# Kernel optimization log

Measured on AMD Instinct MI355X. Metric: run time of the kernel, lower is better.

## Reference

```python
import jax, jax.numpy as jnp
import numpy as np

H = 1024      # hidden_size
NH = 16       # num_attention_heads
KV = 4        # num_key_value_heads
HD = 64       # head_dim
E = 16        # num_experts
K = 2         # num_experts_per_tok
F = 1024      # moe_intermediate_size
EPS = 1e-6
THETA = 10000.0
B, S = 2, 1024


def rmsnorm(x, w):
    v = x.astype(jnp.float32)
    v = v * jax.lax.rsqrt(jnp.mean(v * v, axis=-1, keepdims=True) + EPS)
    return (v * w).astype(x.dtype)


def rotate_half(x):
    h = x.shape[-1] // 2
    return jnp.concatenate([-x[..., h:], x[..., :h]], axis=-1)


def setup_inputs() -> dict:
    key = jax.random.key(0)
    ks = jax.random.split(key, 12)
    s = 0.02
    return {
        "hidden_states": jax.random.normal(ks[0], (B, S, H), jnp.float32),
        "position_ids": jnp.broadcast_to(jnp.arange(S, dtype=jnp.int32), (B, S)),
        "ln1_w": jnp.ones((H,), jnp.float32),
        "ln2_w": jnp.ones((H,), jnp.float32),
        "q_w": jax.random.normal(ks[1], (NH * HD, H), jnp.float32) * s,
        "k_w": jax.random.normal(ks[2], (KV * HD, H), jnp.float32) * s,
        "v_w": jax.random.normal(ks[3], (KV * HD, H), jnp.float32) * s,
        "o_w": jax.random.normal(ks[4], (H, NH * HD), jnp.float32) * s,
        "qn_w": jnp.ones((HD,), jnp.float32),
        "kn_w": jnp.ones((HD,), jnp.float32),
        "gate_w": jax.random.normal(ks[5], (E, H), jnp.float32) * s,
        "w_gate": jax.random.normal(ks[6], (E, F, H), jnp.float32) * s,
        "w_up": jax.random.normal(ks[7], (E, F, H), jnp.float32) * s,
        "w_down": jax.random.normal(ks[8], (E, H, F), jnp.float32) * s,
    }


def reference(hidden_states, position_ids, ln1_w, ln2_w, q_w, k_w, v_w, o_w,
              qn_w, kn_w, gate_w, w_gate, w_up, w_down):
    b, s, _ = hidden_states.shape
    # ---- attention (pre-norm, bidirectional, GQA, RoPE, q/k RMSNorm) ----
    h = rmsnorm(hidden_states, ln1_w)
    q = (h @ q_w.T).reshape(b, s, NH, HD)
    k = (h @ k_w.T).reshape(b, s, KV, HD)
    v = (h @ v_w.T).reshape(b, s, KV, HD)
    q = jnp.swapaxes(rmsnorm(q, qn_w), 1, 2)   # [b,NH,s,HD]
    k = jnp.swapaxes(rmsnorm(k, kn_w), 1, 2)   # [b,KV,s,HD]
    v = jnp.swapaxes(v, 1, 2)
    inv_freq = 1.0 / (THETA ** (jnp.arange(0, HD, 2, dtype=jnp.float32) / HD))
    freqs = position_ids.astype(jnp.float32)[..., None] * inv_freq  # [b,s,HD/2]
    emb = jnp.concatenate([freqs, freqs], axis=-1)                  # [b,s,HD]
    cos = jnp.cos(emb)[:, None]                                     # [b,1,s,HD]
    sin = jnp.sin(emb)[:, None]
    q = q * cos + rotate_half(q) * sin
    k = k * cos + rotate_half(k) * sin
    rep = NH // KV
    k = jnp.repeat(k, rep, axis=1)
    v = jnp.repeat(v, rep, axis=1)
    scores = jnp.einsum('bhqd,bhkd->bhqk', q, k) * (HD ** -0.5)
    attn = jax.nn.softmax(scores.astype(jnp.float32), axis=-1).astype(q.dtype)
    o = jnp.einsum('bhqk,bhkd->bhqd', attn, v)
    o = jnp.swapaxes(o, 1, 2).reshape(b, s, NH * HD) @ o_w.T
    x1 = hidden_states + o
    # ---- sparse MoE (pre-norm, top-k routing, silu-gated experts) ----
    h2 = rmsnorm(x1, ln2_w)
    xf = h2.reshape(-1, H)                                  # [T,H]
    logits = xf @ gate_w.T                                  # [T,E]
    probs = jax.nn.softmax(logits.astype(jnp.float32), axis=-1)
    w, sel = jax.lax.top_k(probs, K)                        # [T,K]
    w = w / jnp.sum(w, axis=-1, keepdims=True)              # norm_topk_prob
    T = xf.shape[0]
    # combine weights scattered into dense [T,E] (zero for unselected experts)
    cw = jnp.zeros((T, E), jnp.float32).at[jnp.arange(T)[:, None], sel].add(w)
    g = jnp.einsum('th,efh->tef', xf, w_gate)
    u = jnp.einsum('th,efh->tef', xf, w_up)
    a = jax.nn.silu(g) * u
    y = jnp.einsum('tef,ehf,te->th', a, w_down, cw.astype(xf.dtype))
    out = x1 + y.reshape(b, s, H)
    return out, logits.reshape(b, s, E)
```

## Files before the change

kernel.cpp:

```cpp
#include <hip/hip_runtime.h>
#include <hip/hip_bf16.h>
#include <math.h>

typedef __bf16 bf16x8 __attribute__((ext_vector_type(8)));
typedef float f32x4 __attribute__((ext_vector_type(4)));

constexpr int HID = 1024;
constexpr int NHEAD = 16;
constexpr int NKV = 4;
constexpr int HDIM = 64;
constexpr int NEXP = 16;
constexpr int FFD = 1024;
constexpr int NB = 2;
constexpr int SEQ = 1024;
constexpr int TOK = NB * SEQ;
constexpr int QKV_N = NHEAD * HDIM + 2 * NKV * HDIM;
constexpr float RMS_EPS = 1e-6f;
constexpr int LDP = 32;
constexpr int PL = 64 * LDP;
constexpr int MAXBLK = 2 * TOK / 64 + NEXP;

__device__ __forceinline__ int swz(int row, int e8) {
  return row * LDP + (e8 ^ (((row >> 1) & 3) << 3));
}

__device__ __forceinline__ void split2(float x, __bf16& h1, __bf16& h2) {
  h1 = (__bf16)x;
  h2 = (__bf16)(x - (float)h1);
}

__device__ __forceinline__ void mfma_step3(const __bf16* sm, int wr, int wc,
                                           int lm, int lq, f32x4 (&acc)[2][2]) {
  int ao0 = swz(wr + lm, lq * 8), ao1 = ao0 + 16 * LDP;
  int bo0 = swz(wc + lm, lq * 8), bo1 = bo0 + 16 * LDP;
  bf16x8 a10 = *(const bf16x8*)(sm + ao0),          a11 = *(const bf16x8*)(sm + ao1);
  bf16x8 a20 = *(const bf16x8*)(sm + PL + ao0),     a21 = *(const bf16x8*)(sm + PL + ao1);
  bf16x8 b10 = *(const bf16x8*)(sm + 2 * PL + bo0), b11 = *(const bf16x8*)(sm + 2 * PL + bo1);
  bf16x8 b20 = *(const bf16x8*)(sm + 3 * PL + bo0), b21 = *(const bf16x8*)(sm + 3 * PL + bo1);
#define MF(A, B, i, j) acc[i][j] = __builtin_amdgcn_mfma_f32_16x16x32_bf16(A, B, acc[i][j], 0, 0, 0)
  MF(a10, b10, 0, 0); MF(a10, b11, 0, 1); MF(a11, b10, 1, 0); MF(a11, b11, 1, 1);
  MF(a10, b20, 0, 0); MF(a10, b21, 0, 1); MF(a11, b20, 1, 0); MF(a11, b21, 1, 1);
  MF(a20, b10, 0, 0); MF(a20, b11, 0, 1); MF(a21, b10, 1, 0); MF(a21, b11, 1, 1);
#undef MF
}

__device__ __forceinline__ void cvt8(__bf16* dst, float4 f0, float4 f1) {
  __bf16 tmp[8] __attribute__((aligned(16))) = {
      (__bf16)f0.x, (__bf16)f0.y, (__bf16)f0.z, (__bf16)f0.w,
      (__bf16)f1.x, (__bf16)f1.y, (__bf16)f1.z, (__bf16)f1.w};
  *(int4*)dst = *(const int4*)tmp;
}


__global__ __launch_bounds__(256) void split2_kernel(
    const float* __restrict__ src, __bf16* __restrict__ p1,
    __bf16* __restrict__ p2, int n) {
  int i = (blockIdx.x * 256 + threadIdx.x) * 4;
  if (i >= n) return;
  float4 v = *(const float4*)(src + i);
  __bf16 t1[4] __attribute__((aligned(8))), t2[4] __attribute__((aligned(8)));
  split2(v.x, t1[0], t2[0]);
  split2(v.y, t1[1], t2[1]);
  split2(v.z, t1[2], t2[2]);
  split2(v.w, t1[3], t2[3]);
  *(int2*)(p1 + i) = *(const int2*)t1;
  *(int2*)(p2 + i) = *(const int2*)t2;
}

__global__ __launch_bounds__(256) void rmsnorm_split2_kernel(
    const float* __restrict__ x, const float* __restrict__ w,
    __bf16* __restrict__ p1, __bf16* __restrict__ p2) {
  int row = blockIdx.x;
  const float* xr = x + (size_t)row * HID;
  float4 v = ((const float4*)xr)[threadIdx.x];
  float ss = v.x * v.x + v.y * v.y + v.z * v.z + v.w * v.w;
  for (int off = 32; off; off >>= 1) ss += __shfl_xor(ss, off);
  __shared__ float red[4];
  int lane = threadIdx.x & 63, wid = threadIdx.x >> 6;
  if (lane == 0) red[wid] = ss;
  __syncthreads();
  float tot = red[0] + red[1] + red[2] + red[3];
  float scale = rsqrtf(tot / (float)HID + RMS_EPS);
  float4 wv = ((const float4*)w)[threadIdx.x];
  float o[4] = {v.x * scale * wv.x, v.y * scale * wv.y,
                v.z * scale * wv.z, v.w * scale * wv.w};
  __bf16 t1[4] __attribute__((aligned(8))), t2[4] __attribute__((aligned(8)));
#pragma unroll
  for (int i = 0; i < 4; i++) split2(o[i], t1[i], t2[i]);
  size_t idx = (size_t)row * HID + threadIdx.x * 4;
  *(int2*)(p1 + idx) = *(const int2*)t1;
  *(int2*)(p2 + idx) = *(const int2*)t2;
}

__global__ __launch_bounds__(256) void rmsnorm_dual_kernel(
    const float* __restrict__ x, const float* __restrict__ w,
    float* __restrict__ outf, __bf16* __restrict__ outb) {
  int row = blockIdx.x;
  const float* xr = x + (size_t)row * HID;
  float4 v = ((const float4*)xr)[threadIdx.x];
  float ss = v.x * v.x + v.y * v.y + v.z * v.z + v.w * v.w;
  for (int off = 32; off; off >>= 1) ss += __shfl_xor(ss, off);
  __shared__ float red[4];
  int lane = threadIdx.x & 63, wid = threadIdx.x >> 6;
  if (lane == 0) red[wid] = ss;
  __syncthreads();
  float tot = red[0] + red[1] + red[2] + red[3];
// ... 7 lines not shown
#pragma unroll
  for (int i = 0; i < 4; i++) tb[i] = (__bf16)o[i];
  *(int2*)(outb + idx) = *(const int2*)tb;
}

__global__ __launch_bounds__(256) void rope_split_kernel(
    const float* __restrict__ qkv, const int* __restrict__ pos_ids,
    const float* __restrict__ qn_w, const float* __restrict__ kn_w,
    __bf16* __restrict__ qp1, __bf16* __restrict__ qp2,
    __bf16* __restrict__ kp1, __bf16* __restrict__ kp2,
    __bf16* __restrict__ vp1, __bf16* __restrict__ vp2) {
  int t = blockIdx.x;
  int b = t >> 10, s = t & 1023;
  int lane = threadIdx.x & 63, w = threadIdx.x >> 6;
  float pos = (float)pos_ids[t];
  int fi = lane & 31;
  float inv = powf(10000.0f, -((float)(2 * fi)) / 64.0f);
  float cs = cosf(pos * inv), sn = sinf(pos * inv);
  for (int i = 0; i < 6; i++) {
    int hh = w + 4 * i;
    float val = qkv[(size_t)t * QKV_N + hh * 64 + lane];
    __bf16 h1, h2;
    if (hh < 20) {
      float ss = val * val;
      for (int off = 32; off; off >>= 1) ss += __shfl_xor(ss, off);
      float scale = rsqrtf(ss / 64.0f + RMS_EPS);
      float wgt = (hh < 16) ? qn_w[lane] : kn_w[lane];
      val = val * scale * wgt;
      float partner = __shfl_xor(val, 32);
      float rot = (lane < 32) ? -partner : partner;
      val = val * cs + rot * sn;
      split2(val, h1, h2);
      if (hh < 16) {
        size_t idx = (((size_t)b * NHEAD + hh) * SEQ + s) * HDIM + lane;
        qp1[idx] = h1; qp2[idx] = h2;
      } else {
        size_t idx = (((size_t)b * NKV + (hh - 16)) * SEQ + s) * HDIM + lane;
        kp1[idx] = h1; kp2[idx] = h2;
      }
    } else {
      split2(val, h1, h2);
      size_t idx = (((size_t)b * NKV + (hh - 20)) * HDIM + lane) * SEQ + s;
      vp1[idx] = h1; vp2[idx] = h2;
    }
  }
}

__global__ __launch_bounds__(256) void softmax2_kernel(
    const float* __restrict__ sf,
    __bf16* __restrict__ p1, __bf16* __restrict__ p2) {
  size_t roff = (size_t)blockIdx.x * SEQ;
  int tid = threadIdx.x;
  float4 v4 = *(const float4*)(sf + roff + tid * 4);
  float v[4] = {v4.x, v4.y, v4.z, v4.w};
  float mx = fmaxf(fmaxf(v[0], v[1]), fmaxf(v[2], v[3]));
  for (int off = 32; off; off >>= 1) mx = fmaxf(mx, __shfl_xor(mx, off));
  __shared__ float red[4], red2[4];
  int lane = tid & 63, wid = tid >> 6;
  if (lane == 0) red[wid] = mx;
  __syncthreads();
  mx = fmaxf(fmaxf(red[0], red[1]), fmaxf(red[2], red[3]));
  float e[4], sum = 0.f;
#pragma unroll
  for (int i = 0; i < 4; i++) { e[i] = expf(v[i] - mx); sum += e[i]; }
  for (int off = 32; off; off >>= 1) sum += __shfl_xor(sum, off);
  if (lane == 0) red2[wid] = sum;
  __syncthreads();
  sum = red2[0] + red2[1] + red2[2] + red2[3];
  float invs = 1.0f / sum;
  __bf16 t1[4] __attribute__((aligned(8))), t2[4] __attribute__((aligned(8)));
#pragma unroll
  for (int i = 0; i < 4; i++) split2(e[i] * invs, t1[i], t2[i]);
  *(int2*)(p1 + roff + tid * 4) = *(const int2*)t1;
  *(int2*)(p2 + roff + tid * 4) = *(const int2*)t2;
}


__global__ __launch_bounds__(256) void gemm_qkv4(
    const __bf16* __restrict__ a1, const __bf16* __restrict__ a2,
    const __bf16* __restrict__ b1, const __bf16* __restrict__ b2,
    float* __restrict__ qkv) {
  int m0 = blockIdx.x * 64, n0 = blockIdx.y * 64;
  __shared__ __bf16 sm[2][4 * PL];
  int tid = threadIdx.x, r = tid >> 2, c8 = (tid & 3) * 8;
  size_t aoff = (size_t)(m0 + r) * HID + c8, boff = (size_t)(n0 + r) * HID + c8;
  f32x4 acc[2][2] = {};
  int lane = tid & 63, wid = tid >> 6;
  int wr = (wid >> 1) * 32, wc = (wid & 1) * 32, lq = lane >> 4, lm = lane & 15;
  int sidx = swz(r, c8);
  int4 rA1, rA2, rA3, rA4, rB1, rB2, rB3, rB4;
  auto preloadA = [&](int k0) {
    rA1 = *(const int4*)(a1 + aoff + k0); rA2 = *(const int4*)(a2 + aoff + k0);
    rA3 = *(const int4*)(b1 + boff + k0); rA4 = *(const int4*)(b2 + boff + k0);
  };
  auto preloadB = [&](int k0) {
    rB1 = *(const int4*)(a1 + aoff + k0); rB2 = *(const int4*)(a2 + aoff + k0);
    rB3 = *(const int4*)(b1 + boff + k0); rB4 = *(const int4*)(b2 + boff + k0);
  };
  auto stageA = [&](int p) {
    *(int4*)&sm[p][0 * PL + sidx] = rA1; *(int4*)&sm[p][1 * PL + sidx] = rA2;
    *(int4*)&sm[p][2 * PL + sidx] = rA3; *(int4*)&sm[p][3 * PL + sidx] = rA4;
  };
  auto stageB = [&](int p) {
    *(int4*)&sm[p][0 * PL + sidx] = rB1; *(int4*)&sm[p][1 * PL + sidx] = rB2;
    *(int4*)&sm[p][2 * PL + sidx] = rB3; *(int4*)&sm[p][3 * PL + sidx] = rB4;
  };
  preloadA(0); stageA(0);
  preloadA(32); preloadB(64);
  __syncthreads();
  int p = 0;
  for (int k0 = 0; k0 < HID; k0 += 64) {
    if (k0 + 32 < HID) stageA(p ^ 1);
    if (k0 + 96 < HID) preloadA(k0 + 96);
    mfma_step3(sm[p], wr, wc, lm, lq, acc);
    __syncthreads(); p ^= 1;
    if (k0 + 64 < HID) stageB(p ^ 1);
    if (k0 + 128 < HID) preloadB(k0 + 128);
    mfma_step3(sm[p], wr, wc, lm, lq, acc);
    __syncthreads(); p ^= 1;
  }
#pragma unroll
  for (int mt = 0; mt < 2; mt++)
#pragma unroll
    for (int nt = 0; nt < 2; nt++)
#pragma unroll
      for (int i = 0; i < 4; i++) {
        int gm = m0 + wr + mt * 16 + lq * 4 + i;
        int gc = n0 + wc + nt * 16 + lm;
        qkv[(size_t)gm * QKV_N + gc] = acc[mt][nt][i];
      }
}

__global__ __launch_bounds__(256) void gemm_scores4(
    const __bf16* __restrict__ qp1, const __bf16* __restrict__ qp2,
    const __bf16* __restrict__ kp1, const __bf16* __restrict__ kp2,
    float* __restrict__ sf, int b, int h0) {
  int hz = blockIdx.z, h = h0 + hz;
  int m0 = blockIdx.x * 64, n0 = blockIdx.y * 64;
  size_t qbase = ((size_t)(b * NHEAD + h)) * SEQ * HDIM;
  size_t kbase = ((size_t)(b * NKV + (h >> 2))) * SEQ * HDIM;
  __shared__ __bf16 sm[4 * PL];
  int tid = threadIdx.x, r = tid >> 2, c8 = (tid & 3) * 8;
  size_t aoff = qbase + (size_t)(m0 + r) * HDIM + c8;
  size_t boff = kbase + (size_t)(n0 + r) * HDIM + c8;
  f32x4 acc[2][2] = {};
  int lane = tid & 63, wid = tid >> 6;
  int wr = (wid >> 1) * 32, wc = (wid & 1) * 32, lq = lane >> 4, lm = lane & 15;
  int sidx = swz(r, c8);
  int4 ra1, ra2, rb1, rb2;
  auto preload = [&](int k0) {
    ra1 = *(const int4*)(qp1 + aoff + k0);
    ra2 = *(const int4*)(qp2 + aoff + k0);
    rb1 = *(const int4*)(kp1 + boff + k0);
    rb2 = *(const int4*)(kp2 + boff + k0);
  };
  auto stage = [&]() {
    *(int4*)&sm[0 * PL + sidx] = ra1;
    *(int4*)&sm[1 * PL + sidx] = ra2;
    *(int4*)&sm[2 * PL + sidx] = rb1;
    *(int4*)&sm[3 * PL + sidx] = rb2;
  };
  preload(0); stage();
  for (int k0 = 0; k0 < HDIM; k0 += 32) {
    __syncthreads();
    if (k0 + 32 < HDIM) preload(k0 + 32);
    mfma_step3(sm, wr, wc, lm, lq, acc);
    __syncthreads();
    if (k0 + 32 < HDIM) stage();
  }
#pragma unroll
  for (int mt = 0; mt < 2; mt++)
#pragma unroll
    for (int nt = 0; nt < 2; nt++)
#pragma unroll
      for (int i = 0; i < 4; i++) {
        int gm = m0 + wr + mt * 16 + lq * 4 + i;
        int gc = n0 + wc + nt * 16 + lm;
        size_t idx = ((size_t)hz * SEQ + gm) * SEQ + gc;
        sf[idx] = acc[mt][nt][i] * 0.125f;
      }
}

__global__ __launch_bounds__(256) void gemm_pv4(
    const __bf16* __restrict__ s1, const __bf16* __restrict__ s2,
    const __bf16* __restrict__ vp1, const __bf16* __restrict__ vp2,
    __bf16* __restrict__ o1, __bf16* __restrict__ o2,
    int b, int h0) {
  int hz = blockIdx.z, h = h0 + hz;
  int m0 = blockIdx.x * 64;
  size_t pbase = (size_t)hz * SEQ * SEQ;
  size_t vbase = ((size_t)(b * NKV + (h >> 2))) * HDIM * SEQ;
  __shared__ __bf16 sm[2][4 * PL];
  int tid = threadIdx.x, r = tid >> 2, c8 = (tid & 3) * 8;
  size_t aoff = pbase + (size_t)(m0 + r) * SEQ + c8;
  size_t boff = vbase + (size_t)r * SEQ + c8;
  f32x4 acc[2][2] = {};
  int lane = tid & 63, wid = tid >> 6;
  int wr = (wid >> 1) * 32, wc = (wid & 1) * 32, lq = lane >> 4, lm = lane & 15;
  int sidx = swz(r, c8);
  int4 rA1, rA2, rA3, rA4, rB1, rB2, rB3, rB4;
  auto preloadA = [&](int k0) {
    rA1 = *(const int4*)(s1 + aoff + k0);  rA2 = *(const int4*)(s2 + aoff + k0);
    rA3 = *(const int4*)(vp1 + boff + k0); rA4 = *(const int4*)(vp2 + boff + k0);
  };
  auto preloadB = [&](int k0) {
    rB1 = *(const int4*)(s1 + aoff + k0);  rB2 = *(const int4*)(s2 + aoff + k0);
    rB3 = *(const int4*)(vp1 + boff + k0); rB4 = *(const int4*)(vp2 + boff + k0);
  };
  auto stageA = [&](int p) {
    *(int4*)&sm[p][0 * PL + sidx] = rA1; *(int4*)&sm[p][1 * PL + sidx] = rA2;
    *(int4*)&sm[p][2 * PL + sidx] = rA3; *(int4*)&sm[p][3 * PL + sidx] = rA4;
  };
  auto stageB = [&](int p) {
    *(int4*)&sm[p][0 * PL + sidx] = rB1; *(int4*)&sm[p][1 * PL + sidx] = rB2;
    *(int4*)&sm[p][2 * PL + sidx] = rB3; *(int4*)&sm[p][3 * PL + sidx] = rB4;
  };
  preloadA(0); stageA(0);
  preloadA(32); preloadB(64);
  __syncthreads();
  int p = 0;
  for (int k0 = 0; k0 < SEQ; k0 += 64) {
    if (k0 + 32 < SEQ) stageA(p ^ 1);
    if (k0 + 96 < SEQ) preloadA(k0 + 96);
    mfma_step3(sm[p], wr, wc, lm, lq, acc);
    __syncthreads(); p ^= 1;
    if (k0 + 64 < SEQ) stageB(p ^ 1);
    if (k0 + 128 < SEQ) preloadB(k0 + 128);
    mfma_step3(sm[p], wr, wc, lm, lq, acc);
    __syncthreads(); p ^= 1;
  }
#pragma unroll
  for (int mt = 0; mt < 2; mt++)
#pragma unroll
    for (int nt = 0; nt < 2; nt++)
#pragma unroll
      for (int i = 0; i < 4; i++) {
        int gm = m0 + wr + mt * 16 + lq * 4 + i;
        int gc = wc + nt * 16 + lm;
        size_t idx = ((size_t)(b * SEQ + gm)) * HID + h * 64 + gc;
        __bf16 h1_, h2_;
        split2(acc[mt][nt][i], h1_, h2_);
        o1[idx] = h1_; o2[idx] = h2_;
      }
}

__global__ __launch_bounds__(256) void gemm_oproj4(
    const __bf16* __restrict__ a1, const __bf16* __restrict__ a2,
    const __bf16* __restrict__ b1, const __bf16* __restrict__ b2,
    const float* __restrict__ hidden, float* __restrict__ x1, float* __restrict__ outp) {
  int m0 = blockIdx.x * 64, n0 = blockIdx.y * 64;
  __shared__ __bf16 sm[2][4 * PL];
  int tid = threadIdx.x, r = tid >> 2, c8 = (tid & 3) * 8;
  size_t aoff = (size_t)(m0 + r) * HID + c8, boff = (size_t)(n0 + r) * HID + c8;
  f32x4 acc[2][2] = {};
  int lane = tid & 63, wid = tid >> 6;
  int wr = (wid >> 1) * 32, wc = (wid & 1) * 32, lq = lane >> 4, lm = lane & 15;
  int sidx = swz(r, c8);
  int4 rA1, rA2, rA3, rA4, rB1, rB2, rB3, rB4;
  auto preloadA = [&](int k0) {
    rA1 = *(const int4*)(a1 + aoff + k0); rA2 = *(const int4*)(a2 + aoff + k0);
    rA3 = *(const int4*)(b1 + boff + k0); rA4 = *(const int4*)(b2 + boff + k0);
  };
  auto preloadB = [&](int k0) {
    rB1 = *(const int4*)(a1 + aoff + k0); rB2 = *(const int4*)(a2 + aoff + k0);
    rB3 = *(const int4*)(b1 + boff + k0); rB4 = *(const int4*)(b2 + boff + k0);
  };
  auto stageA = [&](int p) {
    *(int4*)&sm[p][0 * PL + sidx] = rA1; *(int4*)&sm[p][1 * PL + sidx] = rA2;
    *(int4*)&sm[p][2 * PL + sidx] = rA3; *(int4*)&sm[p][3 * PL + sidx] = rA4;
  };
  auto stageB = [&](int p) {
    *(int4*)&sm[p][0 * PL + sidx] = rB1; *(int4*)&sm[p][1 * PL + sidx] = rB2;
    *(int4*)&sm[p][2 * PL + sidx] = rB3; *(int4*)&sm[p][3 * PL + sidx] = rB4;
  };
  preloadA(0); stageA(0);
  preloadA(32); preloadB(64);
  __syncthreads();
  int p = 0;
  for (int k0 = 0; k0 < HID; k0 += 64) {
    if (k0 + 32 < HID) stageA(p ^ 1);
    if (k0 + 96 < HID) preloadA(k0 + 96);
    mfma_step3(sm[p], wr, wc, lm, lq, acc);
    __syncthreads(); p ^= 1;
    if (k0 + 64 < HID) stageB(p ^ 1);
    if (k0 + 128 < HID) preloadB(k0 + 128);
    mfma_step3(sm[p], wr, wc, lm, lq, acc);
    __syncthreads(); p ^= 1;
  }
#pragma unroll
  for (int mt = 0; mt < 2; mt++)
#pragma unroll
    for (int nt = 0; nt < 2; nt++)
#pragma unroll
      for (int i = 0; i < 4; i++) {
        int gm = m0 + wr + mt * 16 + lq * 4 + i;
        int gc = n0 + wc + nt * 16 + lm;
        size_t idx = (size_t)gm * HID + gc;
        float val = hidden[idx] + acc[mt][nt][i];
        x1[idx] = val;
        outp[idx] = val;
      }
}


__global__ void zero_cnt_kernel(int* cnt) {
  if (threadIdx.x < NEXP) cnt[threadIdx.x] = 0;
}

__global__ __launch_bounds__(64) void gating_kernel(
    const float* __restrict__ h2f, const float* __restrict__ gw,
    float* __restrict__ logits_out, int* __restrict__ cnt,
    int* __restrict__ list, float* __restrict__ wt) {
  int t = blockIdx.x;
  int lane = threadIdx.x;
  const float* xr = h2f + (size_t)t * HID;
  float part[NEXP] = {};
  for (int k = lane; k < HID; k += 64) {
    float xv = xr[k];
#pragma unroll
    for (int e = 0; e < NEXP; e++) part[e] += xv * gw[e * HID + k];
  }
#pragma unroll
  for (int e = 0; e < NEXP; e++)
    for (int off = 32; off; off >>= 1) part[e] += __shfl_xor(part[e], off);
  if (lane < NEXP) logits_out[(size_t)t * NEXP + lane] = part[lane];
  float mx = part[0];
#pragma unroll
  for (int e = 1; e < NEXP; e++) mx = fmaxf(mx, part[e]);
  float pe[NEXP];
#pragma unroll
  for (int e = 0; e < NEXP; e++) pe[e] = expf(part[e] - mx);
  int e0 = 0; float p0 = pe[0];
#pragma unroll
  for (int e = 1; e < NEXP; e++) if (pe[e] > p0) { p0 = pe[e]; e0 = e; }
  int e1 = -1; float p1 = -1.f;
#pragma unroll
  for (int e = 0; e < NEXP; e++) if (e != e0 && pe[e] > p1) { p1 = pe[e]; e1 = e; }
  float wsum = p0 + p1;
  if (lane == 0) {
    int pos0 = atomicAdd(&cnt[e0], 1);
    list[e0 * TOK + pos0] = t;
    wt[e0 * TOK + pos0] = p0 / wsum;
    int pos1 = atomicAdd(&cnt[e1], 1);
    list[e1 * TOK + pos1] = t;
    wt[e1 * TOK + pos1] = p1 / wsum;
  }
}

__global__ void scan_kernel(const int* __restrict__ cnt, int* __restrict__ base,
                            int* __restrict__ btab, int* __restrict__ nblk) {
  if (threadIdx.x == 0 && blockIdx.x == 0) {
    int acc = 0, nb = 0;
    for (int e = 0; e < NEXP; e++) {
      base[e] = acc; acc += cnt[e];
      for (int m0 = 0; m0 < cnt[e]; m0 += 64) {
        btab[2 * nb] = e; btab[2 * nb + 1] = m0; nb++;
      }
    }
    base[NEXP] = acc;
    *nblk = nb;
  }
}

__global__ __launch_bounds__(256) void gemm_gateup3(
    const __bf16* __restrict__ h2, const float* __restrict__ w_gate,
    const float* __restrict__ w_up, const int* __restrict__ cnt,
    const int* __restrict__ base, const int* __restrict__ list,
    const int* __restrict__ btab, const int* __restrict__ nblk,
    __bf16* __restrict__ aws) {
  int slot = blockIdx.y;
  if (slot >= *nblk) return;
  int e = btab[2 * slot], m0 = btab[2 * slot + 1];
  int ce = cnt[e];
  int n0 = blockIdx.x * 64;
  int be = base[e];
  __shared__ __bf16 As[2][PL], Bg[2][PL], Bu[2][PL];
  int tid = threadIdx.x, r = tid >> 2, c8 = (tid & 3) * 8;
  int ridx = m0 + r; if (ridx >= ce) ridx = ce - 1;
  const __bf16* arow = h2 + (size_t)list[e * TOK + ridx] * HID + c8;
  const float* bgrow = w_gate + ((size_t)e * FFD + n0 + r) * HID + c8;
  const float* burow = w_up + ((size_t)e * FFD + n0 + r) * HID + c8;
  int lane = tid & 63, wid = tid >> 6;
  int wr = (wid >> 1) * 32, wc = (wid & 1) * 32, lq = lane >> 4, lm = lane & 15;
  int sidx = swz(r, c8);
  f32x4 ag[2][2] = {}, au[2][2] = {};
  int4 raA, raB; float4 rgA0, rgA1, ruA0, ruA1, rgB0, rgB1, ruB0, ruB1;
  auto preloadA = [&](int k0) {
    raA = *(const int4*)(arow + k0);
    rgA0 = *(const float4*)(bgrow + k0); rgA1 = *(const float4*)(bgrow + k0 + 4);
    ruA0 = *(const float4*)(burow + k0); ruA1 = *(const float4*)(burow + k0 + 4);
  };
  auto preloadB = [&](int k0) {
    raB = *(const int4*)(arow + k0);
    rgB0 = *(const float4*)(bgrow + k0); rgB1 = *(const float4*)(bgrow + k0 + 4);
    ruB0 = *(const float4*)(burow + k0); ruB1 = *(const float4*)(burow + k0 + 4);
  };
  auto stageA = [&](int p) {
    *(int4*)&As[p][sidx] = raA;
    cvt8(&Bg[p][sidx], rgA0, rgA1);
    cvt8(&Bu[p][sidx], ruA0, ruA1);
  };
  auto stageB = [&](int p) {
    *(int4*)&As[p][sidx] = raB;
    cvt8(&Bg[p][sidx], rgB0, rgB1);
    cvt8(&Bu[p][sidx], ruB0, ruB1);
  };
  auto compute = [&](int p) {
    int ao0 = swz(wr + lm, lq * 8), ao1 = ao0 + 16 * LDP;
    int bo0 = swz(wc + lm, lq * 8), bo1 = bo0 + 16 * LDP;
    bf16x8 a0 = *(const bf16x8*)(&As[p][ao0]);
    bf16x8 a1 = *(const bf16x8*)(&As[p][ao1]);
    bf16x8 g0 = *(const bf16x8*)(&Bg[p][bo0]);
    bf16x8 g1 = *(const bf16x8*)(&Bg[p][bo1]);
    bf16x8 u0 = *(const bf16x8*)(&Bu[p][bo0]);
    bf16x8 u1 = *(const bf16x8*)(&Bu[p][bo1]);
    ag[0][0] = __builtin_amdgcn_mfma_f32_16x16x32_bf16(a0, g0, ag[0][0], 0, 0, 0);
    ag[0][1] = __builtin_amdgcn_mfma_f32_16x16x32_bf16(a0, g1, ag[0][1], 0, 0, 0);
    ag[1][0] = __builtin_amdgcn_mfma_f32_16x16x32_bf16(a1, g0, ag[1][0], 0, 0, 0);
    ag[1][1] = __builtin_amdgcn_mfma_f32_16x16x32_bf16(a1, g1, ag[1][1], 0, 0, 0);
    au[0][0] = __builtin_amdgcn_mfma_f32_16x16x32_bf16(a0, u0, au[0][0], 0, 0, 0);
    au[0][1] = __builtin_amdgcn_mfma_f32_16x16x32_bf16(a0, u1, au[0][1], 0, 0, 0);
    au[1][0] = __builtin_amdgcn_mfma_f32_16x16x32_bf16(a1, u0, au[1][0], 0, 0, 0);
    au[1][1] = __builtin_amdgcn_mfma_f32_16x16x32_bf16(a1, u1, au[1][1], 0, 0, 0);
  };
  preloadA(0); stageA(0);
  preloadA(32); preloadB(64);
  __syncthreads();
  int p = 0;
  for (int k0 = 0; k0 < HID; k0 += 64) {
    if (k0 + 32 < HID) stageA(p ^ 1);
    if (k0 + 96 < HID) preloadA(k0 + 96);
    compute(p);
    __syncthreads(); p ^= 1;
    if (k0 + 64 < HID) stageB(p ^ 1);
    if (k0 + 128 < HID) preloadB(k0 + 128);
    compute(p);
    __syncthreads(); p ^= 1;
  }
#pragma unroll
  for (int mt = 0; mt < 2; mt++)
#pragma unroll
    for (int nt = 0; nt < 2; nt++)
#pragma unroll
      for (int i = 0; i < 4; i++) {
        int lrow = m0 + wr + mt * 16 + lq * 4 + i;
        if (lrow < ce) {
          int gc = n0 + wc + nt * 16 + lm;
          float g = ag[mt][nt][i], u = au[mt][nt][i];
          float a = g / (1.0f + expf(-g)) * u;
          aws[((size_t)(be + lrow)) * FFD + gc] = (__bf16)a;
        }
      }
}

__global__ __launch_bounds__(256) void gemm_down3(
    const __bf16* __restrict__ aws, const float* __restrict__ w_down,
    const int* __restrict__ cnt, const int* __restrict__ base,
    const int* __restrict__ list, const float* __restrict__ wt,
    const int* __restrict__ btab, const int* __restrict__ nblk,
    float* __restrict__ outp) {
  int slot = blockIdx.y;
  if (slot >= *nblk) return;
  int e = btab[2 * slot], m0 = btab[2 * slot + 1];
  int ce = cnt[e];
  int n0 = blockIdx.x * 64;
  int be = base[e];
  __shared__ __bf16 As[2][PL], Bs[2][PL];
  int tid = threadIdx.x, r = tid >> 2, c8 = (tid & 3) * 8;
  int ridx = m0 + r; if (ridx >= ce) ridx = ce - 1;
  const __bf16* arow = aws + (size_t)(be + ridx) * FFD + c8;
  const float* brow = w_down + ((size_t)e * HID + n0 + r) * FFD + c8;
  int lane = tid & 63, wid = tid >> 6;
  int wr = (wid >> 1) * 32, wc = (wid & 1) * 32, lq = lane >> 4, lm = lane & 15;
  int sidx = swz(r, c8);
  f32x4 acc[2][2] = {};
  int4 raA, raB; float4 rbA0, rbA1, rbB0, rbB1;
  auto preloadA = [&](int k0) {
    raA = *(const int4*)(arow + k0);
    rbA0 = *(const float4*)(brow + k0); rbA1 = *(const float4*)(brow + k0 + 4);
  };
  auto preloadB = [&](int k0) {
    raB = *(const int4*)(arow + k0);
    rbB0 = *(const float4*)(brow + k0); rbB1 = *(const float4*)(brow + k0 + 4);
  };
  auto stageA = [&](int p) {
    *(int4*)&As[p][sidx] = raA;
    cvt8(&Bs[p][sidx], rbA0, rbA1);
  };
  auto stageB = [&](int p) {
    *(int4*)&As[p][sidx] = raB;
    cvt8(&Bs[p][sidx], rbB0, rbB1);
  };
  auto compute = [&](int p) {
    int ao0 = swz(wr + lm, lq * 8), ao1 = ao0 + 16 * LDP;
    int bo0 = swz(wc + lm, lq * 8), bo1 = bo0 + 16 * LDP;
    bf16x8 a0 = *(const bf16x8*)(&As[p][ao0]);
    bf16x8 a1 = *(const bf16x8*)(&As[p][ao1]);
    bf16x8 b0 = *(const bf16x8*)(&Bs[p][bo0]);
    bf16x8 b1 = *(const bf16x8*)(&Bs[p][bo1]);
    acc[0][0] = __builtin_amdgcn_mfma_f32_16x16x32_bf16(a0, b0, acc[0][0], 0, 0, 0);
    acc[0][1] = __builtin_amdgcn_mfma_f32_16x16x32_bf16(a0, b1, acc[0][1], 0, 0, 0);
    acc[1][0] = __builtin_amdgcn_mfma_f32_16x16x32_bf16(a1, b0, acc[1][0], 0, 0, 0);
    acc[1][1] = __builtin_amdgcn_mfma_f32_16x16x32_bf16(a1, b1, acc[1][1], 0, 0, 0);
  };
  preloadA(0); stageA(0);
  preloadA(32); preloadB(64);
  __syncthreads();
  int p = 0;
  for (int k0 = 0; k0 < FFD; k0 += 64) {
    if (k0 + 32 < FFD) stageA(p ^ 1);
    if (k0 + 96 < FFD) preloadA(k0 + 96);
    compute(p);
    __syncthreads(); p ^= 1;
    if (k0 + 64 < FFD) stageB(p ^ 1);
    if (k0 + 128 < FFD) preloadB(k0 + 128);
    compute(p);
    __syncthreads(); p ^= 1;
  }
#pragma unroll
  for (int mt = 0; mt < 2; mt++)
#pragma unroll
    for (int nt = 0; nt < 2; nt++)
#pragma unroll
      for (int i = 0; i < 4; i++) {
        int lrow = m0 + wr + mt * 16 + lq * 4 + i;
        if (lrow < ce) {
          int gc = n0 + wc + nt * 16 + lm;
          int tok = list[e * TOK + lrow];
          float wgt = wt[e * TOK + lrow];
          atomicAdd(&outp[(size_t)tok * HID + gc], wgt * acc[mt][nt][i]);
        }
      }
}


extern "C" void kernel_launch(void* const* d_in, const int* in_sizes, int n_in,
                              void* d_out, int out_size, void* d_ws, size_t ws_size,
                              hipStream_t stream) {
  const float* hidden = (const float*)d_in[0];
  const int* pos_ids = (const int*)d_in[1];
  const float* ln1_w = (const float*)d_in[2];
  const float* ln2_w = (const float*)d_in[3];
  const float* q_w = (const float*)d_in[4];
  const float* k_w = (const float*)d_in[5];
  const float* v_w = (const float*)d_in[6];
  const float* o_w = (const float*)d_in[7];
  const float* qn_w = (const float*)d_in[8];
  const float* kn_w = (const float*)d_in[9];
  const float* gate_w = (const float*)d_in[10];
  const float* w_gate = (const float*)d_in[11];
  const float* w_up = (const float*)d_in[12];
  const float* w_down = (const float*)d_in[13];
  float* outp = (float*)d_out;
  float* logits_out = outp + (size_t)TOK * HID;

  char* ws = (char*)d_ws;
  size_t off = 0;
  auto alloc = [&](size_t bytes) {
    void* p = ws + off;
    off += (bytes + 255) & ~(size_t)255;
    return p;
  };
  const size_t NWQ = (size_t)QKV_N * HID, NOW = (size_t)HID * HID;
  __bf16* wqp1 = (__bf16*)alloc(NWQ * 2); __bf16* wqp2 = (__bf16*)alloc(NWQ * 2);
  __bf16* owp1 = (__bf16*)alloc(NOW * 2); __bf16* owp2 = (__bf16*)alloc(NOW * 2);
  const size_t NH1 = (size_t)TOK * HID;
  __bf16* h1p1 = (__bf16*)alloc(NH1 * 2); __bf16* h1p2 = (__bf16*)alloc(NH1 * 2);
  float* qkvf = (float*)alloc((size_t)TOK * QKV_N * 4);
  const size_t NQ = (size_t)NB * NHEAD * SEQ * HDIM, NK = (size_t)NB * NKV * SEQ * HDIM;
  __bf16* qp1 = (__bf16*)alloc(NQ * 2); __bf16* qp2 = (__bf16*)alloc(NQ * 2);
  __bf16* kp1 = (__bf16*)alloc(NK * 2); __bf16* kp2 = (__bf16*)alloc(NK * 2);
  __bf16* vp1 = (__bf16*)alloc(NK * 2); __bf16* vp2 = (__bf16*)alloc(NK * 2);
  size_t fixed_rest = NH1 * 2 * 2  + NH1 * 4 * 2  + NH1 * 2  +
                      NEXP * 4 * 2 + (size_t)NEXP * TOK * 8 +
                      (size_t)TOK * 2 * FFD * 2 + (1 << 20);
  size_t avail = (ws_size > off + fixed_rest) ? (ws_size - off - fixed_rest) : 0;
  int hch = (avail >= (size_t)16 * SEQ * SEQ * 8) ? 16 : 8;
  const size_t NP = (size_t)hch * SEQ * SEQ;
  float* spf = (float*)alloc(NP * 4);
  __bf16* sp1 = (__bf16*)alloc(NP * 2); __bf16* sp2 = (__bf16*)alloc(NP * 2);
  __bf16* op1 = (__bf16*)alloc(NH1 * 2); __bf16* op2 = (__bf16*)alloc(NH1 * 2);
  float* x1 = (float*)alloc(NH1 * 4);
  float* h2f = (float*)alloc(NH1 * 4);
  __bf16* h2b = (__bf16*)alloc(NH1 * 2);
  int* cnt = (int*)alloc(NEXP * 4);
  int* base = (int*)alloc((NEXP + 1) * 4);
  int* list = (int*)alloc((size_t)NEXP * TOK * 4);
  float* wt = (float*)alloc((size_t)NEXP * TOK * 4);
  int* btab = (int*)alloc((size_t)MAXBLK * 2 * 4);
  int* nblk = (int*)alloc(4);
  __bf16* aws = (__bf16*)alloc((size_t)TOK * 2 * FFD * 2);
  (void)in_sizes; (void)n_in; (void)out_size;

  split2_kernel<<<1024, 256, 0, stream>>>(q_w, wqp1, wqp2, 1024 * 1024);
  split2_kernel<<<256, 256, 0, stream>>>(k_w, wqp1 + 1024 * 1024, wqp2 + 1024 * 1024,
                                         256 * 1024);
  split2_kernel<<<256, 256, 0, stream>>>(v_w, wqp1 + 1280 * 1024, wqp2 + 1280 * 1024,
                                         256 * 1024);
  split2_kernel<<<1024, 256, 0, stream>>>(o_w, owp1, owp2, 1024 * 1024);

  rmsnorm_split2_kernel<<<TOK, 256, 0, stream>>>(hidden, ln1_w, h1p1, h1p2);
  gemm_qkv4<<<dim3(TOK / 64, QKV_N / 64), 256, 0, stream>>>(
      h1p1, h1p2, wqp1, wqp2, qkvf);
// ... 24 lines not shown
```

Measured before the change: 533.3 us.

## Use direct global-to-LDS loads in GEMMs and widen MoE expert tiles to 128 rows

All bf16 GEMM operand tiles (qkv, scores, pv, o-proj, and the activation side of the MoE gate/up and down kernels) are now loaded with global_load_lds. The swizzle is applied on the global address side, so data no longer passes through registers before the LDS store. The MoE expert kernels also move from 64-row to 128-row token tiles, with each wave computing 4x2 MFMA tiles. This halves the number of expert block slots and doubles reuse of each fp32 weight tile converted to bf16. The trade-offs are higher register and LDS use in the MoE kernels, more padded rows for experts with few tokens, and a simpler single-stage double buffer whose correctness depends on the async LDS writes being complete at the barrier.

```diff
diff --git a/kernel.cpp b/kernel.cpp
--- a/kernel.cpp
+++ b/kernel.cpp
@@ -18,10 +18,16 @@
 constexpr float RMS_EPS = 1e-6f;
 constexpr int LDP = 32;
 constexpr int PL = 64 * LDP;
-constexpr int MAXBLK = 2 * TOK / 64 + NEXP;
+constexpr int MAXBLK = 2 * TOK / 128 + NEXP;
 
 __device__ __forceinline__ int swz(int row, int e8) {
   return row * LDP + (e8 ^ (((row >> 1) & 3) << 3));
+}
+
+__device__ __forceinline__ void gload_lds16(const void* g, void* l) {
+  __builtin_amdgcn_global_load_lds(
+      (const __attribute__((address_space(1))) void*)g,
+      (__attribute__((address_space(3))) void*)l, 16, 0, 0);
 }
 
 __device__ __forceinline__ void split2(float x, __bf16& h1, __bf16& h2) {
@@ -195,42 +201,25 @@
     float* __restrict__ qkv) {
   int m0 = blockIdx.x * 64, n0 = blockIdx.y * 64;
   __shared__ __bf16 sm[2][4 * PL];
-  int tid = threadIdx.x, r = tid >> 2, c8 = (tid & 3) * 8;
-  size_t aoff = (size_t)(m0 + r) * HID + c8, boff = (size_t)(n0 + r) * HID + c8;
+  int tid = threadIdx.x, r = tid >> 2;
+  int csw = ((tid & 3) ^ ((r >> 1) & 3)) * 8;
+  size_t aoff = (size_t)(m0 + r) * HID + csw, boff = (size_t)(n0 + r) * HID + csw;
   f32x4 acc[2][2] = {};
   int lane = tid & 63, wid = tid >> 6;
   int wr = (wid >> 1) * 32, wc = (wid & 1) * 32, lq = lane >> 4, lm = lane & 15;
-  int sidx = swz(r, c8);
-  int4 rA1, rA2, rA3, rA4, rB1, rB2, rB3, rB4;
-  auto preloadA = [&](int k0) {
-    rA1 = *(const int4*)(a1 + aoff + k0); rA2 = *(const int4*)(a2 + aoff + k0);
-    rA3 = *(const int4*)(b1 + boff + k0); rA4 = *(const int4*)(b2 + boff + k0);
-  };
-  auto preloadB = [&](int k0) {
-    rB1 = *(const int4*)(a1 + aoff + k0); rB2 = *(const int4*)(a2 + aoff + k0);
-    rB3 = *(const int4*)(b1 + boff + k0); rB4 = *(const int4*)(b2 + boff + k0);
-  };
-  auto stageA = [&](int p) {
-    *(int4*)&sm[p][0 * PL + sidx] = rA1; *(int4*)&sm[p][1 * PL + sidx] = rA2;
-    *(int4*)&sm[p][2 * PL + sidx] = rA3; *(int4*)&sm[p][3 * PL + sidx] = rA4;
-  };
-  auto stageB = [&](int p) {
-    *(int4*)&sm[p][0 * PL + sidx] = rB1; *(int4*)&sm[p][1 * PL + sidx] = rB2;
-    *(int4*)&sm[p][2 * PL + sidx] = rB3; *(int4*)&sm[p][3 * PL + sidx] = rB4;
-  };
-  preloadA(0); stageA(0);
-  preloadA(32); preloadB(64);
+  auto gld4 = [&](int p, int k0) {
+    gload_lds16(a1 + aoff + k0, &sm[p][0 * PL + tid * 8]);
+    gload_lds16(a2 + aoff + k0, &sm[p][1 * PL + tid * 8]);
+    gload_lds16(b1 + boff + k0, &sm[p][2 * PL + tid * 8]);
+    gload_lds16(b2 + boff + k0, &sm[p][3 * PL + tid * 8]);
+  };
+  gld4(0, 0);
   __syncthreads();
   int p = 0;
-  for (int k0 = 0; k0 < HID; k0 += 64) {
-    if (k0 + 32 < HID) stageA(p ^ 1);
-    if (k0 + 96 < HID) preloadA(k0 + 96);
+  for (int k0 = 0; k0 < HID; k0 += 32, p ^= 1) {
+    if (k0 + 32 < HID) gld4(p ^ 1, k0 + 32);
     mfma_step3(sm[p], wr, wc, lm, lq, acc);
-    __syncthreads(); p ^= 1;
-    if (k0 + 64 < HID) stageB(p ^ 1);
-    if (k0 + 128 < HID) preloadB(k0 + 128);
-    mfma_step3(sm[p], wr, wc, lm, lq, acc);
-    __syncthreads(); p ^= 1;
+    __syncthreads();
   }
 #pragma unroll
   for (int mt = 0; mt < 2; mt++)
@@ -252,34 +241,27 @@
   int m0 = blockIdx.x * 64, n0 = blockIdx.y * 64;
   size_t qbase = ((size_t)(b * NHEAD + h)) * SEQ * HDIM;
   size_t kbase = ((size_t)(b * NKV + (h >> 2))) * SEQ * HDIM;
-  __shared__ __bf16 sm[4 * PL];
-  int tid = threadIdx.x, r = tid >> 2, c8 = (tid & 3) * 8;
-  size_t aoff = qbase + (size_t)(m0 + r) * HDIM + c8;
-  size_t boff = kbase + (size_t)(n0 + r) * HDIM + c8;
+  __shared__ __bf16 sm[2][4 * PL];
+  int tid = threadIdx.x, r = tid >> 2;
+  int csw = ((tid & 3) ^ ((r >> 1) & 3)) * 8;
+  size_t aoff = qbase + (size_t)(m0 + r) * HDIM + csw;
+  size_t boff = kbase + (size_t)(n0 + r) * HDIM + csw;
   f32x4 acc[2][2] = {};
   int lane = tid & 63, wid = tid >> 6;
   int wr = (wid >> 1) * 32, wc = (wid & 1) * 32, lq = lane >> 4, lm = lane & 15;
-  int sidx = swz(r, c8);
-  int4 ra1, ra2, rb1, rb2;
-  auto preload = [&](int k0) {
-    ra1 = *(const int4*)(qp1 + aoff + k0);
-    ra2 = *(const int4*)(qp2 + aoff + k0);
-    rb1 = *(const int4*)(kp1 + boff + k0);
-    rb2 = *(const int4*)(kp2 + boff + k0);
-  };
-  auto stage = [&]() {
-    *(int4*)&sm[0 * PL + sidx] = ra1;
-    *(int4*)&sm[1 * PL + sidx] = ra2;
-    *(int4*)&sm[2 * PL + sidx] = rb1;
-    *(int4*)&sm[3 * PL + sidx] = rb2;
-  };
-  preload(0); stage();
-  for (int k0 = 0; k0 < HDIM; k0 += 32) {
+  auto gld4 = [&](int p, int k0) {
+    gload_lds16(qp1 + aoff + k0, &sm[p][0 * PL + tid * 8]);
+    gload_lds16(qp2 + aoff + k0, &sm[p][1 * PL + tid * 8]);
+    gload_lds16(kp1 + boff + k0, &sm[p][2 * PL + tid * 8]);
+    gload_lds16(kp2 + boff + k0, &sm[p][3 * PL + tid * 8]);
+  };
+  gld4(0, 0);
+  __syncthreads();
+  int p = 0;
+  for (int k0 = 0; k0 < HDIM; k0 += 32, p ^= 1) {
+    if (k0 + 32 < HDIM) gld4(p ^ 1, k0 + 32);
+    mfma_step3(sm[p], wr, wc, lm, lq, acc);
     __syncthreads();
-    if (k0 + 32 < HDIM) preload(k0 + 32);
-    mfma_step3(sm, wr, wc, lm, lq, acc);
-    __syncthreads();
-    if (k0 + 32 < HDIM) stage();
   }
 #pragma unroll
   for (int mt = 0; mt < 2; mt++)
@@ -304,43 +286,26 @@
   size_t pbase = (size_t)hz * SEQ * SEQ;
   size_t vbase = ((size_t)(b * NKV + (h >> 2))) * HDIM * SEQ;
   __shared__ __bf16 sm[2][4 * PL];
-  int tid = threadIdx.x, r = tid >> 2, c8 = (tid & 3) * 8;
-  size_t aoff = pbase + (size_t)(m0 + r) * SEQ + c8;
-  size_t boff = vbase + (size_t)r * SEQ + c8;
+  int tid = threadIdx.x, r = tid >> 2;
+  int csw = ((tid & 3) ^ ((r >> 1) & 3)) * 8;
+  size_t aoff = pbase + (size_t)(m0 + r) * SEQ + csw;
+  size_t boff = vbase + (size_t)r * SEQ + csw;
   f32x4 acc[2][2] = {};
   int lane = tid & 63, wid = tid >> 6;
   int wr = (wid >> 1) * 32, wc = (wid & 1) * 32, lq = lane >> 4, lm = lane & 15;
-  int sidx = swz(r, c8);
-  int4 rA1, rA2, rA3, rA4, rB1, rB2, rB3, rB4;
-  auto preloadA = [&](int k0) {
-    rA1 = *(const int4*)(s1 + aoff + k0);  rA2 = *(const int4*)(s2 + aoff + k0);
-    rA3 = *(const int4*)(vp1 + boff + k0); rA4 = *(const int4*)(vp2 + boff + k0);
-  };
-  auto preloadB = [&](int k0) {
-    rB1 = *(const int4*)(s1 + aoff + k0);  rB2 = *(const int4*)(s2 + aoff + k0);
-    rB3 = *(const int4*)(vp1 + boff + k0); rB4 = *(const int4*)(vp2 + boff + k0);
-  };
-  auto stageA = [&](int p) {
-    *(int4*)&sm[p][0 * PL + sidx] = rA1; *(int4*)&sm[p][1 * PL + sidx] = rA2;
-    *(int4*)&sm[p][2 * PL + sidx] = rA3; *(int4*)&sm[p][3 * PL + sidx] = rA4;
-  };
-  auto stageB = [&](int p) {
-    *(int4*)&sm[p][0 * PL + sidx] = rB1; *(int4*)&sm[p][1 * PL + sidx] = rB2;
-    *(int4*)&sm[p][2 * PL + sidx] = rB3; *(int4*)&sm[p][3 * PL + sidx] = rB4;
-  };
-  preloadA(0); stageA(0);
-  preloadA(32); preloadB(64);
+  auto gld4 = [&](int p, int k0) {
+    gload_lds16(s1 + aoff + k0, &sm[p][0 * PL + tid * 8]);
+    gload_lds16(s2 + aoff + k0, &sm[p][1 * PL + tid * 8]);
+    gload_lds16(vp1 + boff + k0, &sm[p][2 * PL + tid * 8]);
+    gload_lds16(vp2 + boff + k0, &sm[p][3 * PL + tid * 8]);
+  };
+  gld4(0, 0);
   __syncthreads();
   int p = 0;
-  for (int k0 = 0; k0 < SEQ; k0 += 64) {
-    if (k0 + 32 < SEQ) stageA(p ^ 1);
-    if (k0 + 96 < SEQ) preloadA(k0 + 96);
+  for (int k0 = 0; k0 < SEQ; k0 += 32, p ^= 1) {
+    if (k0 + 32 < SEQ) gld4(p ^ 1, k0 + 32);
     mfma_step3(sm[p], wr, wc, lm, lq, acc);
-    __syncthreads(); p ^= 1;
-    if (k0 + 64 < SEQ) stageB(p ^ 1);
-    if (k0 + 128 < SEQ) preloadB(k0 + 128);
-    mfma_step3(sm[p], wr, wc, lm, lq, acc);
-    __syncthreads(); p ^= 1;
+    __syncthreads();
   }
 #pragma unroll
   for (int mt = 0; mt < 2; mt++)
@@ -363,42 +328,25 @@
     const float* __restrict__ hidden, float* __restrict__ x1, float* __restrict__ outp) {
   int m0 = blockIdx.x * 64, n0 = blockIdx.y * 64;
   __shared__ __bf16 sm[2][4 * PL];
-  int tid = threadIdx.x, r = tid >> 2, c8 = (tid & 3) * 8;
-  size_t aoff = (size_t)(m0 + r) * HID + c8, boff = (size_t)(n0 + r) * HID + c8;
+  int tid = threadIdx.x, r = tid >> 2;
+  int csw = ((tid & 3) ^ ((r >> 1) & 3)) * 8;
+  size_t aoff = (size_t)(m0 + r) * HID + csw, boff = (size_t)(n0 + r) * HID + csw;
   f32x4 acc[2][2] = {};
   int lane = tid & 63, wid = tid >> 6;
   int wr = (wid >> 1) * 32, wc = (wid & 1) * 32, lq = lane >> 4, lm = lane & 15;
-  int sidx = swz(r, c8);
-  int4 rA1, rA2, rA3, rA4, rB1, rB2, rB3, rB4;
-  auto preloadA = [&](int k0) {
-    rA1 = *(const int4*)(a1 + aoff + k0); rA2 = *(const int4*)(a2 + aoff + k0);
-    rA3 = *(const int4*)(b1 + boff + k0); rA4 = *(const int4*)(b2 + boff + k0);
-  };
-  auto preloadB = [&](int k0) {
-    rB1 = *(const int4*)(a1 + aoff + k0); rB2 = *(const int4*)(a2 + aoff + k0);
-    rB3 = *(const int4*)(b1 + boff + k0); rB4 = *(const int4*)(b2 + boff + k0);
-  };
-  auto stageA = [&](int p) {
-    *(int4*)&sm[p][0 * PL + sidx] = rA1; *(int4*)&sm[p][1 * PL + sidx] = rA2;
-    *(int4*)&sm[p][2 * PL + sidx] = rA3; *(int4*)&sm[p][3 * PL + sidx] = rA4;
-  };
-  auto stageB = [&](int p) {
-    *(int4*)&sm[p][0 * PL + sidx] = rB1; *(int4*)&sm[p][1 * PL + sidx] = rB2;
-    *(int4*)&sm[p][2 * PL + sidx] = rB3; *(int4*)&sm[p][3 * PL + sidx] = rB4;
-  };
-  preloadA(0); stageA(0);
-  preloadA(32); preloadB(64);
+  auto gld4 = [&](int p, int k0) {
+    gload_lds16(a1 + aoff + k0, &sm[p][0 * PL + tid * 8]);
+    gload_lds16(a2 + aoff + k0, &sm[p][1 * PL + tid * 8]);
+    gload_lds16(b1 + boff + k0, &sm[p][2 * PL + tid * 8]);
+    gload_lds16(b2 + boff + k0, &sm[p][3 * PL + tid * 8]);
+  };
+  gld4(0, 0);
   __syncthreads();
   int p = 0;
-  for (int k0 = 0; k0 < HID; k0 += 64) {
-    if (k0 + 32 < HID) stageA(p ^ 1);
-    if (k0 + 96 < HID) preloadA(k0 + 96);
+  for (int k0 = 0; k0 < HID; k0 += 32, p ^= 1) {
+    if (k0 + 32 < HID) gld4(p ^ 1, k0 + 32);
     mfma_step3(sm[p], wr, wc, lm, lq, acc);
-    __syncthreads(); p ^= 1;
-    if (k0 + 64 < HID) stageB(p ^ 1);
-    if (k0 + 128 < HID) preloadB(k0 + 128);
-    mfma_step3(sm[p], wr, wc, lm, lq, acc);
-    __syncthreads(); p ^= 1;
+    __syncthreads();
   }
 #pragma unroll
   for (int mt = 0; mt < 2; mt++)
@@ -466,7 +414,7 @@
     int acc = 0, nb = 0;
     for (int e = 0; e < NEXP; e++) {
       base[e] = acc; acc += cnt[e];
-      for (int m0 = 0; m0 < cnt[e]; m0 += 64) {
+      for (int m0 = 0; m0 < cnt[e]; m0 += 128) {
         btab[2 * nb] = e; btab[2 * nb + 1] = m0; nb++;
       }
     }
@@ -487,71 +435,64 @@
   int ce = cnt[e];
   int n0 = blockIdx.x * 64;
   int be = base[e];
-  __shared__ __bf16 As[2][PL], Bg[2][PL], Bu[2][PL];
+  __shared__ __bf16 As[2][128 * LDP], Bg[2][PL], Bu[2][PL];
   int tid = threadIdx.x, r = tid >> 2, c8 = (tid & 3) * 8;
-  int ridx = m0 + r; if (ridx >= ce) ridx = ce - 1;
-  const __bf16* arow = h2 + (size_t)list[e * TOK + ridx] * HID + c8;
+  int csw = ((tid & 3) ^ ((r >> 1) & 3)) * 8;
+  int rx0 = m0 + r;      if (rx0 >= ce) rx0 = ce - 1;
+  int rx1 = m0 + 64 + r; if (rx1 >= ce) rx1 = ce - 1;
+  const __bf16* arow0 = h2 + (size_t)list[e * TOK + rx0] * HID + csw;
+  const __bf16* arow1 = h2 + (size_t)list[e * TOK + rx1] * HID + csw;
   const float* bgrow = w_gate + ((size_t)e * FFD + n0 + r) * HID + c8;
   const float* burow = w_up + ((size_t)e * FFD + n0 + r) * HID + c8;
   int lane = tid & 63, wid = tid >> 6;
-  int wr = (wid >> 1) * 32, wc = (wid & 1) * 32, lq = lane >> 4, lm = lane & 15;
+  int wr = (wid >> 1) * 64, wc = (wid & 1) * 32, lq = lane >> 4, lm = lane & 15;
   int sidx = swz(r, c8);
-  f32x4 ag[2][2] = {}, au[2][2] = {};
-  int4 raA, raB; float4 rgA0, rgA1, ruA0, ruA1, rgB0, rgB1, ruB0, ruB1;
-  auto preloadA = [&](int k0) {
-    raA = *(const int4*)(arow + k0);
-    rgA0 = *(const float4*)(bgrow + k0); rgA1 = *(const float4*)(bgrow + k0 + 4);
-    ruA0 = *(const float4*)(burow + k0); ruA1 = *(const float4*)(burow + k0 + 4);
+  f32x4 ag[4][2] = {}, au[4][2] = {};
+  float4 rg0, rg1, ru0, ru1;
+  auto gldA = [&](int p, int k0) {
+    gload_lds16(arow0 + k0, &As[p][tid * 8]);
+    gload_lds16(arow1 + k0, &As[p][2048 + tid * 8]);
   };
   auto preloadB = [&](int k0) {
-    raB = *(const int4*)(arow + k0);
-    rgB0 = *(const float4*)(bgrow + k0); rgB1 = *(const float4*)(bgrow + k0 + 4);
-    ruB0 = *(const float4*)(burow + k0); ruB1 = *(const float4*)(burow + k0 + 4);
-  };
-  auto stageA = [&](int p) {
-    *(int4*)&As[p][sidx] = raA;
-    cvt8(&Bg[p][sidx], rgA0, rgA1);
-    cvt8(&Bu[p][sidx], ruA0, ruA1);
+    rg0 = *(const float4*)(bgrow + k0); rg1 = *(const float4*)(bgrow + k0 + 4);
+    ru0 = *(const float4*)(burow + k0); ru1 = *(const float4*)(burow + k0 + 4);
   };
   auto stageB = [&](int p) {
-    *(int4*)&As[p][sidx] = raB;
-    cvt8(&Bg[p][sidx], rgB0, rgB1);
-    cvt8(&Bu[p][sidx], ruB0, ruB1);
+    cvt8(&Bg[p][sidx], rg0, rg1);
+    cvt8(&Bu[p][sidx], ru0, ru1);
   };
   auto compute = [&](int p) {
-    int ao0 = swz(wr + lm, lq * 8), ao1 = ao0 + 16 * LDP;
     int bo0 = swz(wc + lm, lq * 8), bo1 = bo0 + 16 * LDP;
-    bf16x8 a0 = *(const bf16x8*)(&As[p][ao0]);
-    bf16x8 a1 = *(const bf16x8*)(&As[p][ao1]);
     bf16x8 g0 = *(const bf16x8*)(&Bg[p][bo0]);
     bf16x8 g1 = *(const bf16x8*)(&Bg[p][bo1]);
     bf16x8 u0 = *(const bf16x8*)(&Bu[p][bo0]);
     bf16x8 u1 = *(const bf16x8*)(&Bu[p][bo1]);
-    ag[0][0] = __builtin_amdgcn_mfma_f32_16x16x32_bf16(a0, g0, ag[0][0], 0, 0, 0);
-    ag[0][1] = __builtin_amdgcn_mfma_f32_16x16x32_bf16(a0, g1, ag[0][1], 0, 0, 0);
-    ag[1][0] = __builtin_amdgcn_mfma_f32_16x16x32_bf16(a1, g0, ag[1][0], 0, 0, 0);
-    ag[1][1] = __builtin_amdgcn_mfma_f32_16x16x32_bf16(a1, g1, ag[1][1], 0, 0, 0);
-    au[0][0] = __builtin_amdgcn_mfma_f32_16x16x32_bf16(a0, u0, au[0][0], 0, 0, 0);
-    au[0][1] = __builtin_amdgcn_mfma_f32_16x16x32_bf16(a0, u1, au[0][1], 0, 0, 0);
-    au[1][0] = __builtin_amdgcn_mfma_f32_16x16x32_bf16(a1, u0, au[1][0], 0, 0, 0);
-    au[1][1] = __builtin_amdgcn_mfma_f32_16x16x32_bf16(a1, u1, au[1][1], 0, 0, 0);
-  };
-  preloadA(0); stageA(0);
-  preloadA(32); preloadB(64);
+#pragma unroll
+    for (int mt = 0; mt < 4; mt++) {
+      bf16x8 a = *(const bf16x8*)(&As[p][swz(wr + mt * 16 + lm, lq * 8)]);
+      ag[mt][0] = __builtin_amdgcn_mfma_f32_16x16x32_bf16(a, g0, ag[mt][0], 0, 0, 0);
+      ag[mt][1] = __builtin_amdgcn_mfma_f32_16x16x32_bf16(a, g1, ag[mt][1], 0, 0, 0);
+      au[mt][0] = __builtin_amdgcn_mfma_f32_16x16x32_bf16(a, u0, au[mt][0], 0, 0, 0);
+      au[mt][1] = __builtin_amdgcn_mfma_f32_16x16x32_bf16(a, u1, au[mt][1], 0, 0, 0);
+    }
+  };
+  preloadB(0);
+  gldA(0, 0);
+  stageB(0);
+  preloadB(32);
   __syncthreads();
   int p = 0;
-  for (int k0 = 0; k0 < HID; k0 += 64) {
-    if (k0 + 32 < HID) stageA(p ^ 1);
-    if (k0 + 96 < HID) preloadA(k0 + 96);
+  for (int k0 = 0; k0 < HID; k0 += 32, p ^= 1) {
+    if (k0 + 32 < HID) {
+      gldA(p ^ 1, k0 + 32);
+      stageB(p ^ 1);
+      preloadB(k0 + 64 < HID ? k0 + 64 : 0);
+    }
     compute(p);
-    __syncthreads(); p ^= 1;
-    if (k0 + 64 < HID) stageB(p ^ 1);
-    if (k0 + 128 < HID) preloadB(k0 + 128);
-    compute(p);
-    __syncthreads(); p ^= 1;
-  }
-#pragma unroll
-  for (int mt = 0; mt < 2; mt++)
+    __syncthreads();
+  }
+#pragma unroll
+  for (int mt = 0; mt < 4; mt++)
 #pragma unroll
     for (int nt = 0; nt < 2; nt++)
 #pragma unroll
@@ -578,60 +519,55 @@
   int ce = cnt[e];
   int n0 = blockIdx.x * 64;
   int be = base[e];
-  __shared__ __bf16 As[2][PL], Bs[2][PL];
+  __shared__ __bf16 As[2][128 * LDP], Bs[2][PL];
   int tid = threadIdx.x, r = tid >> 2, c8 = (tid & 3) * 8;
-  int ridx = m0 + r; if (ridx >= ce) ridx = ce - 1;
-  const __bf16* arow = aws + (size_t)(be + ridx) * FFD + c8;
+  int csw = ((tid & 3) ^ ((r >> 1) & 3)) * 8;
+  int rx0 = m0 + r;      if (rx0 >= ce) rx0 = ce - 1;
+  int rx1 = m0 + 64 + r; if (rx1 >= ce) rx1 = ce - 1;
+  const __bf16* arow0 = aws + (size_t)(be + rx0) * FFD + csw;
+  const __bf16* arow1 = aws + (size_t)(be + rx1) * FFD + csw;
   const float* brow = w_down + ((size_t)e * HID + n0 + r) * FFD + c8;
   int lane = tid & 63, wid = tid >> 6;
-  int wr = (wid >> 1) * 32, wc = (wid & 1) * 32, lq = lane >> 4, lm = lane & 15;
+  int wr = (wid >> 1) * 64, wc = (wid & 1) * 32, lq = lane >> 4, lm = lane & 15;
   int sidx = swz(r, c8);
-  f32x4 acc[2][2] = {};
-  int4 raA, raB; float4 rbA0, rbA1, rbB0, rbB1;
-  auto preloadA = [&](int k0) {
-    raA = *(const int4*)(arow + k0);
-    rbA0 = *(const float4*)(brow + k0); rbA1 = *(const float4*)(brow + k0 + 4);
+  f32x4 acc[4][2] = {};
+  float4 rb0, rb1;
+  auto gldA = [&](int p, int k0) {
+    gload_lds16(arow0 + k0, &As[p][tid * 8]);
+    gload_lds16(arow1 + k0, &As[p][2048 + tid * 8]);
   };
   auto preloadB = [&](int k0) {
-    raB = *(const int4*)(arow + k0);
-    rbB0 = *(const float4*)(brow + k0); rbB1 = *(const float4*)(brow + k0 + 4);
-  };
-  auto stageA = [&](int p) {
-    *(int4*)&As[p][sidx] = raA;
-    cvt8(&Bs[p][sidx], rbA0, rbA1);
-  };
-  auto stageB = [&](int p) {
-    *(int4*)&As[p][sidx] = raB;
-    cvt8(&Bs[p][sidx], rbB0, rbB1);
-  };
+    rb0 = *(const float4*)(brow + k0); rb1 = *(const float4*)(brow + k0 + 4);
+  };
+  auto stageB = [&](int p) { cvt8(&Bs[p][sidx], rb0, rb1); };
   auto compute = [&](int p) {
-    int ao0 = swz(wr + lm, lq * 8), ao1 = ao0 + 16 * LDP;
     int bo0 = swz(wc + lm, lq * 8), bo1 = bo0 + 16 * LDP;
-    bf16x8 a0 = *(const bf16x8*)(&As[p][ao0]);
-    bf16x8 a1 = *(const bf16x8*)(&As[p][ao1]);
     bf16x8 b0 = *(const bf16x8*)(&Bs[p][bo0]);
     bf16x8 b1 = *(const bf16x8*)(&Bs[p][bo1]);
-    acc[0][0] = __builtin_amdgcn_mfma_f32_16x16x32_bf16(a0, b0, acc[0][0], 0, 0, 0);
-    acc[0][1] = __builtin_amdgcn_mfma_f32_16x16x32_bf16(a0, b1, acc[0][1], 0, 0, 0);
-    acc[1][0] = __builtin_amdgcn_mfma_f32_16x16x32_bf16(a1, b0, acc[1][0], 0, 0, 0);
-    acc[1][1] = __builtin_amdgcn_mfma_f32_16x16x32_bf16(a1, b1, acc[1][1], 0, 0, 0);
-  };
-  preloadA(0); stageA(0);
-  preloadA(32); preloadB(64);
+#pragma unroll
+    for (int mt = 0; mt < 4; mt++) {
+      bf16x8 a = *(const bf16x8*)(&As[p][swz(wr + mt * 16 + lm, lq * 8)]);
+      acc[mt][0] = __builtin_amdgcn_mfma_f32_16x16x32_bf16(a, b0, acc[mt][0], 0, 0, 0);
+      acc[mt][1] = __builtin_amdgcn_mfma_f32_16x16x32_bf16(a, b1, acc[mt][1], 0, 0, 0);
+    }
+  };
+  preloadB(0);
+  gldA(0, 0);
+  stageB(0);
+  preloadB(32);
   __syncthreads();
   int p = 0;
-  for (int k0 = 0; k0 < FFD; k0 += 64) {
-    if (k0 + 32 < FFD) stageA(p ^ 1);
-    if (k0 + 96 < FFD) preloadA(k0 + 96);
+  for (int k0 = 0; k0 < FFD; k0 += 32, p ^= 1) {
+    if (k0 + 32 < FFD) {
+      gldA(p ^ 1, k0 + 32);
+      stageB(p ^ 1);
+      preloadB(k0 + 64 < FFD ? k0 + 64 : 0);
+    }
     compute(p);
-    __syncthreads(); p ^= 1;
-    if (k0 + 64 < FFD) stageB(p ^ 1);
-    if (k0 + 128 < FFD) preloadB(k0 + 128);
-    compute(p);
-    __syncthreads(); p ^= 1;
-  }
-#pragma unroll
-  for (int mt = 0; mt < 2; mt++)
+    __syncthreads();
+  }
+#pragma unroll
+  for (int mt = 0; mt < 4; mt++)
 #pragma unroll
     for (int nt = 0; nt < 2; nt++)
 #pragma unroll
```

Result: no change. 531.9 us (-0.3%).
